# Kernel tuning notes

Measured on AMD Instinct MI355X. Metric: run time of the kernel, lower is better.

The kernel has to match this reference:

```python
import jax, jax.numpy as jnp
import numpy as np

N_NODES = 50000
N_EDGES = 600000
IN_CH, HID, EMB = 128, 128, 64


def _glorot(key, shape):
    fan_in, fan_out = shape[1], shape[0]
    lim = np.sqrt(6.0 / (fan_in + fan_out))
    return jax.random.uniform(key, shape, jnp.float32, -lim, lim)


def setup_inputs() -> dict:
    key = jax.random.key(0)
    ks = jax.random.split(key, 12)
    x = jax.random.normal(ks[0], (N_NODES, IN_CH), jnp.float32)
    edge_index = jax.random.randint(ks[1], (2, N_EDGES), 0, N_NODES, jnp.int64)
    return {
        "x": x,
        "edge_index": edge_index,
        # SAGEConv layer 1: lin_l (neighbor, with bias) + lin_r (root, no bias)
        "w1n": _glorot(ks[2], (HID, IN_CH)),
        "w1r": _glorot(ks[3], (HID, IN_CH)),
        "b1": jnp.zeros((HID,), jnp.float32),
        "w2n": _glorot(ks[4], (HID, HID)),
        "w2r": _glorot(ks[5], (HID, HID)),
        "b2": jnp.zeros((HID,), jnp.float32),
        "w3n": _glorot(ks[6], (EMB, HID)),
        "w3r": _glorot(ks[7], (EMB, HID)),
        "b3": jnp.zeros((EMB,), jnp.float32),
    }


def _sage_conv(x, src, dst, wn, wr, b):
    # mean aggregation of source-node features at destination nodes
    msg = x[src]                                            # [E, d_in]
    agg = jax.ops.segment_sum(msg, dst, num_segments=N_NODES)
    deg = jax.ops.segment_sum(jnp.ones((src.shape[0],), x.dtype), dst,
                              num_segments=N_NODES)
    agg = agg / jnp.maximum(deg, 1.0)[:, None]
    return agg @ wn.T + x @ wr.T + b


def reference(x, edge_index, w1n, w1r, b1, w2n, w2r, b2, w3n, w3r, b3):
    src, dst = edge_index[0], edge_index[1]
    h = jax.nn.relu(_sage_conv(x, src, dst, w1n, w1r, b1))
    # dropout(p=0.3) is identity in inference mode
    h = jax.nn.relu(_sage_conv(h, src, dst, w2n, w2r, b2))
    h = _sage_conv(h, src, dst, w3n, w3r, b3)
    return h
```

## Files before the change

kernel.cpp:

```cpp
#include <hip/hip_runtime.h>
#include <hip/hip_bf16.h>

#define NN 50000
#define ZROW 50000
#define ELLW 64
#define F8MINDEG 6

#define NB 128
#define BSH 9
#define BCAP 8192
#define EPB 2048

typedef short bf16x8 __attribute__((ext_vector_type(8)));
typedef float f32x4 __attribute__((ext_vector_type(4)));
typedef float floatx2 __attribute__((ext_vector_type(2)));

#if __has_builtin(__builtin_amdgcn_cvt_pk_f32_fp8) && __has_builtin(__builtin_amdgcn_cvt_pk_fp8_f32)
#define HWF8 1
#endif

__device__ __forceinline__ float bf_lo(unsigned int p) {
    union { unsigned int u; float f; } c; c.u = p << 16; return c.f;
}
__device__ __forceinline__ float bf_hi(unsigned int p) {
    union { unsigned int u; float f; } c; c.u = p & 0xffff0000u; return c.f;
}
__device__ __forceinline__ unsigned short bfbits(float f) {
    __hip_bfloat16 h = __float2bfloat16(f);
    union { __hip_bfloat16 b; unsigned short s; } c; c.b = h; return c.s;
}
__device__ __forceinline__ unsigned int pack_bf(float a, float b) {
    return (unsigned int)bfbits(a) | ((unsigned int)bfbits(b) << 16);
}
__device__ __forceinline__ void stv(float* p, float v) { *p = v; }
__device__ __forceinline__ void stv(unsigned short* p, float v) { *p = bfbits(v); }

__device__ __forceinline__ floatx2 bfpair(unsigned int p) {
    union { unsigned int u; float f; } lo, hi;
    lo.u = p << 16; hi.u = p & 0xffff0000u;
    return floatx2{lo.f, hi.f};
}
__device__ __forceinline__ void acc8v(const uint4& u, floatx2* a) {
    a[0] += bfpair(u.x); a[1] += bfpair(u.y);
    a[2] += bfpair(u.z); a[3] += bfpair(u.w);
}

__device__ __forceinline__ unsigned int enc1(float f) {
#ifdef HWF8
    return (unsigned int)__builtin_amdgcn_cvt_pk_fp8_f32(f, f, 0, false) & 0xffu;
#else
    union { float f; unsigned u; } c; c.f = f;
    unsigned s = (c.u >> 24) & 0x80u;
    float af = fabsf(f);
    if (af >= 448.f) return s | 0x7eu;
    if (af < 0.0078125f) {
        unsigned m = (unsigned)(af * 512.f + 0.5f);
        return s | (m > 7u ? 7u : m);
    }
    unsigned u = c.u & 0x7fffffffu;
    u += 0x7ffffu + ((u >> 20) & 1u);
    int e = (int)(u >> 23) - 120;
    if (e < 1) { unsigned m = (unsigned)(af * 512.f + 0.5f); return s | (m > 7u ? 7u : m); }
    if (e > 15) return s | 0x7eu;
    return s | ((unsigned)e << 3) | ((u >> 20) & 7u);
#endif
}
__device__ __forceinline__ unsigned int packf8_4(float x, float y, float z, float w) {
#ifdef HWF8
    int u = __builtin_amdgcn_cvt_pk_fp8_f32(x, y, 0, false);
    u = __builtin_amdgcn_cvt_pk_fp8_f32(z, w, u, true);
    return (unsigned int)u;
#else
    return enc1(x) | (enc1(y) << 8) | (enc1(z) << 16) | (enc1(w) << 24);
#endif
}
__device__ __forceinline__ void accf8v(const uint4& u, floatx2* a) {
#ifdef HWF8
    a[0] += __builtin_amdgcn_cvt_pk_f32_fp8(u.x, false);
    a[1] += __builtin_amdgcn_cvt_pk_f32_fp8(u.x, true);
    a[2] += __builtin_amdgcn_cvt_pk_f32_fp8(u.y, false);
    a[3] += __builtin_amdgcn_cvt_pk_f32_fp8(u.y, true);
    a[4] += __builtin_amdgcn_cvt_pk_f32_fp8(u.z, false);
    a[5] += __builtin_amdgcn_cvt_pk_f32_fp8(u.z, true);
    a[6] += __builtin_amdgcn_cvt_pk_f32_fp8(u.w, false);
    a[7] += __builtin_amdgcn_cvt_pk_f32_fp8(u.w, true);
#else
    const unsigned ww[4] = {u.x, u.y, u.z, u.w};
#pragma unroll
    for (int k = 0; k < 4; k++) {
#pragma unroll
        for (int j = 0; j < 4; j++) {
            unsigned b = (ww[k] >> (8 * j)) & 0xffu;
            unsigned v = ((b & 0x80u) << 24) | (((b & 0x7fu) + (120u << 3)) << 20);
            if ((b & 0x78u) == 0) v = 0u;
            union { unsigned u; float f; } c; c.u = v;
            a[(k * 4 + j) >> 1][(k * 4 + j) & 1] += c.f;
        }
    }
#endif
}

__global__ __launch_bounds__(256) void wb3z_kernel(
    const float* __restrict__ w1n, const float* __restrict__ w1r,
    const float* __restrict__ w2n, const float* __restrict__ w2r,
    const float* __restrict__ w3n, const float* __restrict__ w3r,
    unsigned short* __restrict__ wB1, unsigned short* __restrict__ wB2,
    unsigned short* __restrict__ wB3, int* __restrict__ zblk,
    unsigned short* __restrict__ xb, unsigned short* __restrict__ axc,
    unsigned short* __restrict__ h1b,
    unsigned char* __restrict__ xf8, unsigned char* __restrict__ h1f8) {
    int i = blockIdx.x * blockDim.x + threadIdx.x;
    if (i < 2048) zblk[i] = 0;
    int p = i - 2048;
    if (p >= 0 && p < 256) {
        if (p < 64)       ((unsigned int*)(xb  + (size_t)ZROW * 128))[p] = 0u;
        else if (p < 128) ((unsigned int*)(axc + (size_t)ZROW * 128))[p - 64] = 0u;
        else if (p < 192) ((unsigned int*)(h1b + (size_t)ZROW * 128))[p - 128] = 0u;
        else if (p < 224) ((unsigned int*)(xf8 + (size_t)ZROW * 128))[p - 192] = 0u;
        else              ((unsigned int*)(h1f8 + (size_t)ZROW * 128))[p - 224] = 0u;
    }
    if (i >= 12288) return;
    if (i < 8192) {
        const float* wn = (i < 4096) ? w1n : w2n;
        const float* wr = (i < 4096) ? w1r : w2r;
        unsigned short* wB = (i < 4096) ? wB1 : wB2;
        int li = i & 4095;
        int row = li >> 5;
        int j = (li & 31) * 4;
        float4 a = *(const float4*)(wn + (size_t)row * 128 + j);
        float4 b = *(const float4*)(wr + (size_t)row * 128 + j);
        *(uint2*)(wB + (size_t)row * 256 + j) = uint2{pack_bf(a.x, a.y), pack_bf(a.z, a.w)};
        *(uint2*)(wB + (size_t)row * 256 + 128 + j) = uint2{pack_bf(b.x, b.y), pack_bf(b.z, b.w)};
    } else {
        int li = i - 8192;
        const float* w = (li < 2048) ? w3n : w3r;
        int rbase = (li < 2048) ? 0 : 64;
        int lj = li & 2047;
        int row = lj >> 5;
        int j = (lj & 31) * 4;
        float4 a = *(const float4*)(w + (size_t)row * 128 + j);
        *(uint2*)(wB3 + (size_t)(rbase + row) * 128 + j) =
            uint2{pack_bf(a.x, a.y), pack_bf(a.z, a.w)};
    }
}

__global__ __launch_bounds__(256) void binify_cvt_kernel(
    const float* __restrict__ x,
    unsigned short* __restrict__ xb,
    unsigned char* __restrict__ xf8,
    const int* __restrict__ src,
    const int* __restrict__ dst,
    unsigned int* __restrict__ bpos,
    unsigned int* __restrict__ barr,
    int n4, int E, int nEB) {
    __shared__ int cnt[NB];
    __shared__ int gbase[NB];
    const int t = threadIdx.x;
    const int blk = blockIdx.x;
    if (blk < nEB) {
        int e0 = blk * EPB;
        int ss[8], dd[8], rr[8];
        bool v[8];
#pragma unroll
        for (int k = 0; k < 8; k++) {
            int e = e0 + t + (k << 8);
            v[k] = (e < E);
            ss[k] = v[k] ? src[e] : 0;
            dd[k] = v[k] ? dst[e] : 0;
            rr[k] = 0;
        }
        if (t < NB) cnt[t] = 0;
        __syncthreads();
#pragma unroll
        for (int k = 0; k < 8; k++)
            if (v[k]) rr[k] = atomicAdd(&cnt[dd[k] >> BSH], 1);
        __syncthreads();
        if (t < NB) {
            int c = cnt[t];
            gbase[t] = c ? (int)atomicAdd(&bpos[t], (unsigned)c) : 0;
        }
        __syncthreads();
#pragma unroll
        for (int k = 0; k < 8; k++) {
            if (v[k]) {
                int b = dd[k] >> BSH;
                int pos = gbase[b] + rr[k];
                if (pos < BCAP)
                    barr[b * BCAP + pos] =
                        (unsigned)ss[k] | ((unsigned)dd[k] << 16);
            }
        }
    }
    int gtid = blk * 256 + t;
    int gs = gridDim.x << 8;
    for (int i = gtid; i < n4; i += gs) {
        float4 vv = *(const float4*)(x + 4 * (size_t)i);
        *(uint2*)(xb + 4 * (size_t)i) = uint2{pack_bf(vv.x, vv.y), pack_bf(vv.z, vv.w)};
        *(unsigned int*)(xf8 + 4 * (size_t)i) = packf8_4(vv.x, vv.y, vv.z, vv.w);
    }
}

__global__ __launch_bounds__(256) void ellbuild_kernel(
    const unsigned int* __restrict__ bpos,
    const unsigned int* __restrict__ barr,
    unsigned short* __restrict__ ell,
    int* __restrict__ cnt) {
    __shared__ alignas(16) unsigned short lell[512 * 64];
    __shared__ int lcnt[512];
    const int t = threadIdx.x;
    const int b = blockIdx.x;
    const unsigned PADP = 0xC350C350u;
    for (int i = t; i < 4096; i += 256) ((uint4*)lell)[i] = uint4{PADP, PADP, PADP, PADP};
    for (int i = t; i < 512; i += 256) lcnt[i] = 0;
    __syncthreads();
    int ne = (int)bpos[b];
    if (ne > BCAP) ne = BCAP;
    const unsigned int* seg = barr + (size_t)b * BCAP;
    for (int i = t; i < ne; i += 256) {
        unsigned p = seg[i];
        int ln = (p >> 16) & 511;
        int r = atomicAdd(&lcnt[ln], 1);
        lell[(ln << 6) + (r & (ELLW - 1))] = (unsigned short)(p & 0xffffu);
    }
    __syncthreads();
    int node0 = b << BSH;
    int nn = NN - node0;
    if (nn > 512) nn = 512;
    if (nn <= 0) return;
    uint4* gell = (uint4*)(ell + (size_t)node0 * ELLW);
    const uint4* sell = (const uint4*)lell;
    for (int i = t; i < nn * 8; i += 256) gell[i] = sell[i];
    for (int i = t; i < nn; i += 256) cnt[node0 + i] = lcnt[i];
}

__global__ __launch_bounds__(256) void gather_kernel(
    const int* __restrict__ cnt, const unsigned short* __restrict__ ell,
    const unsigned char* __restrict__ hf8,
    const unsigned short* __restrict__ hb,
    unsigned short* __restrict__ axc,
    int n_nodes) {
    int tid = blockIdx.x * blockDim.x + threadIdx.x;
    int n = tid >> 3;
    if (n >= n_nodes) return;
    int c = (tid & 7) << 4;
    int deg = cnt[n];
    int dd8 = (min(deg, ELLW) + 7) & ~7;
    const unsigned short* cl = ell + (size_t)n * ELLW;
    floatx2 a[8];
#pragma unroll
    for (int k = 0; k < 8; k++) a[k] = floatx2{0.f, 0.f};
    if (deg >= F8MINDEG) {
        for (int i = 0; i < dd8; i += 8) {
            uint4 idv = *(const uint4*)(cl + i);
            int i0 = idv.x & 0xffff, i1 = idv.x >> 16;
            int i2 = idv.y & 0xffff, i3 = idv.y >> 16;
            int i4 = idv.z & 0xffff, i5 = idv.z >> 16;
            int i6 = idv.w & 0xffff, i7 = idv.w >> 16;
            uint4 u0 = *(const uint4*)(hf8 + (size_t)i0 * 128 + c);
            uint4 u1 = *(const uint4*)(hf8 + (size_t)i1 * 128 + c);
            uint4 u2 = *(const uint4*)(hf8 + (size_t)i2 * 128 + c);
            uint4 u3 = *(const uint4*)(hf8 + (size_t)i3 * 128 + c);
            uint4 u4 = *(const uint4*)(hf8 + (size_t)i4 * 128 + c);
            uint4 u5 = *(const uint4*)(hf8 + (size_t)i5 * 128 + c);
            uint4 u6 = *(const uint4*)(hf8 + (size_t)i6 * 128 + c);
            uint4 u7 = *(const uint4*)(hf8 + (size_t)i7 * 128 + c);
            accf8v(u0, a); accf8v(u1, a); accf8v(u2, a); accf8v(u3, a);
            accf8v(u4, a); accf8v(u5, a); accf8v(u6, a); accf8v(u7, a);
        }
    } else {
        for (int i = 0; i < dd8; i += 8) {
            uint4 idv = *(const uint4*)(cl + i);
            int is[8];
            is[0] = idv.x & 0xffff; is[1] = idv.x >> 16;
            is[2] = idv.y & 0xffff; is[3] = idv.y >> 16;
            is[4] = idv.z & 0xffff; is[5] = idv.z >> 16;
            is[6] = idv.w & 0xffff; is[7] = idv.w >> 16;
#pragma unroll
            for (int k = 0; k < 8; k++) {
                uint4 lo = *(const uint4*)(hb + (size_t)is[k] * 128 + c);
                uint4 hi = *(const uint4*)(hb + (size_t)is[k] * 128 + c + 8);
                acc8v(lo, a); acc8v(hi, a + 4);
            }
        }
    }
    float s = 1.0f / (float)max(deg, 1);
    uint4 p0 = {pack_bf(a[0][0] * s, a[0][1] * s), pack_bf(a[1][0] * s, a[1][1] * s),
                pack_bf(a[2][0] * s, a[2][1] * s), pack_bf(a[3][0] * s, a[3][1] * s)};
    uint4 p1 = {pack_bf(a[4][0] * s, a[4][1] * s), pack_bf(a[5][0] * s, a[5][1] * s),
                pack_bf(a[6][0] * s, a[6][1] * s), pack_bf(a[7][0] * s, a[7][1] * s)};
    *(uint4*)(axc + (size_t)n * 128 + c) = p0;
    *(uint4*)(axc + (size_t)n * 128 + c + 8) = p1;
}

__global__ __launch_bounds__(256) void gather_add_kernel(
    const int* __restrict__ cnt, const unsigned short* __restrict__ ell,
    const unsigned short* __restrict__ tu,
    const float* __restrict__ b3,
    float* __restrict__ out, int n_nodes) {
    int tid = blockIdx.x * blockDim.x + threadIdx.x;
    int n = tid >> 3;
    if (n >= n_nodes) return;
    int c = (tid & 7) << 3;
    int deg = cnt[n];
    int dd8 = (min(deg, ELLW) + 7) & ~7;
    const unsigned short* cl = ell + (size_t)n * ELLW;
    floatx2 a[4];
#pragma unroll
    for (int k = 0; k < 4; k++) a[k] = floatx2{0.f, 0.f};
    for (int i = 0; i < dd8; i += 8) {
        uint4 idv = *(const uint4*)(cl + i);
        int i0 = idv.x & 0xffff, i1 = idv.x >> 16;
        int i2 = idv.y & 0xffff, i3 = idv.y >> 16;
        int i4 = idv.z & 0xffff, i5 = idv.z >> 16;
        int i6 = idv.w & 0xffff, i7 = idv.w >> 16;
        uint4 u0 = *(const uint4*)(tu + (size_t)i0 * 128 + c);
        uint4 u1 = *(const uint4*)(tu + (size_t)i1 * 128 + c);
        uint4 u2 = *(const uint4*)(tu + (size_t)i2 * 128 + c);
        uint4 u3 = *(const uint4*)(tu + (size_t)i3 * 128 + c);
        uint4 u4 = *(const uint4*)(tu + (size_t)i4 * 128 + c);
        uint4 u5 = *(const uint4*)(tu + (size_t)i5 * 128 + c);
        uint4 u6 = *(const uint4*)(tu + (size_t)i6 * 128 + c);
        uint4 u7 = *(const uint4*)(tu + (size_t)i7 * 128 + c);
        acc8v(u0, a); acc8v(u1, a); acc8v(u2, a); acc8v(u3, a);
        acc8v(u4, a); acc8v(u5, a); acc8v(u6, a); acc8v(u7, a);
    }
    float s = 1.0f / (float)max(deg, 1);
    uint4 uu = *(const uint4*)(tu + (size_t)n * 128 + 64 + c);
    float4 bA = *(const float4*)(b3 + c);
    float4 bB = *(const float4*)(b3 + c + 4);
    float* o = out + (size_t)n * 64 + c;
    o[0] = a[0][0] * s + bf_lo(uu.x) + bA.x;
    o[1] = a[0][1] * s + bf_hi(uu.x) + bA.y;
    o[2] = a[1][0] * s + bf_lo(uu.y) + bA.z;
    o[3] = a[1][1] * s + bf_hi(uu.y) + bA.w;
    o[4] = a[2][0] * s + bf_lo(uu.z) + bB.x;
    o[5] = a[2][1] * s + bf_hi(uu.z) + bB.y;
    o[6] = a[3][0] * s + bf_lo(uu.w) + bB.z;
    o[7] = a[3][1] * s + bf_hi(uu.w) + bB.w;
}

template <int NKS, bool RELU, bool BIAS, bool F8, typename OUT_T>
__global__ __launch_bounds__(256) void mfma_gemm(
    const unsigned short* __restrict__ A0, const unsigned short* __restrict__ A1,
    const unsigned short* __restrict__ B,
    const float* __restrict__ bias,
    OUT_T* __restrict__ out, unsigned char* __restrict__ f8out,
    int M, int N, int nTilesN) {
    constexpr int KTOT = NKS * 64;
    constexpr int LDB = KTOT + 8;
    __shared__ unsigned short As[2][128 * 72];
    __shared__ unsigned short Bs[64 * LDB];
    const int t = threadIdx.x;
    const int w = t >> 6, l = t & 63;
    const int tileM = blockIdx.x / nTilesN;
    const int n0 = (blockIdx.x - tileM * nTilesN) * 64;
    const int m0 = tileM * 128;
    const int lr = l & 15, lq = l >> 4;

    for (int c = t; c < 64 * (KTOT / 8); c += 256) {
        int row = c / (KTOT / 8);
        int ko = (c - row * (KTOT / 8)) * 8;
        *(uint4*)(&Bs[row * LDB + ko]) =
            *(const uint4*)(&B[(size_t)(n0 + row) * KTOT + ko]);
    }
    for (int c = t; c < 1024; c += 256) {
        int row = c >> 3;
        int ko = (c & 7) * 8;
        int gm = m0 + row;
        uint4 v = {0u, 0u, 0u, 0u};
        if (gm < M) v = *(const uint4*)(A0 + (size_t)gm * 128 + ko);
        *(uint4*)(&As[0][row * 72 + ko]) = v;
    }
    __syncthreads();

    f32x4 acc[2][4];
#pragma unroll
    for (int tm = 0; tm < 2; tm++)
#pragma unroll
        for (int tn = 0; tn < 4; tn++) acc[tm][tn] = f32x4{0.f, 0.f, 0.f, 0.f};

#pragma unroll
    for (int ks = 0; ks < NKS; ks++) {
        uint4 pf[4];
        if (ks + 1 < NKS) {
            int ns = ks + 1;
            const unsigned short* Asrc = (ns < NKS / 2)
                ? (A0 + (size_t)ns * 64) : (A1 + (size_t)(ns - NKS / 2) * 64);
#pragma unroll
            for (int j = 0; j < 4; j++) {
                int c = t + j * 256;
                int row = c >> 3;
                int ko = (c & 7) * 8;
                int gm = m0 + row;
                pf[j] = uint4{0u, 0u, 0u, 0u};
                if (gm < M) pf[j] = *(const uint4*)(Asrc + (size_t)gm * 128 + ko);
            }
        }
        const unsigned short* as = As[ks & 1];
#pragma unroll
        for (int kc = 0; kc < 2; kc++) {
            int lk = kc * 32 + lq * 8;
            bf16x8 af[2], bfr[4];
            af[0] = *(const bf16x8*)(&as[(w * 32 + lr) * 72 + lk]);
            af[1] = *(const bf16x8*)(&as[(w * 32 + 16 + lr) * 72 + lk]);
#pragma unroll
            for (int tn = 0; tn < 4; tn++)
                bfr[tn] = *(const bf16x8*)(&Bs[(tn * 16 + lr) * LDB + ks * 64 + lk]);
#pragma unroll
            for (int tm = 0; tm < 2; tm++)
#pragma unroll
                for (int tn = 0; tn < 4; tn++)
                    acc[tm][tn] = __builtin_amdgcn_mfma_f32_16x16x32_bf16(
                        af[tm], bfr[tn], acc[tm][tn], 0, 0, 0);
        }
        if (ks + 1 < NKS) {
#pragma unroll
            for (int j = 0; j < 4; j++) {
                int c = t + j * 256;
                int row = c >> 3;
                int ko = (c & 7) * 8;
                *(uint4*)(&As[(ks + 1) & 1][row * 72 + ko]) = pf[j];
            }
            __syncthreads();
        }
    }

#pragma unroll
    for (int tn = 0; tn < 4; tn++) {
        int n = n0 + tn * 16 + lr;
        float bj = BIAS ? bias[n] : 0.f;
#pragma unroll
        for (int tm = 0; tm < 2; tm++) {
#pragma unroll
            for (int i = 0; i < 4; i++) {
                int m = m0 + w * 32 + tm * 16 + lq * 4 + i;
                if (m < M) {
                    float v = acc[tm][tn][i] + bj;
                    if (RELU) v = fmaxf(v, 0.f);
                    stv(&out[(size_t)m * N + n], v);
                    if (F8) f8out[(size_t)m * N + n] = (unsigned char)enc1(v);
                }
            }
        }
    }
}

extern "C" void kernel_launch(void* const* d_in, const int* in_sizes, int n_in,
                              void* d_out, int out_size, void* d_ws, size_t ws_size,
                              hipStream_t stream) {
    const float* x  = (const float*)d_in[0];
    const int* ei   = (const int*)d_in[1];
    const float* w1n = (const float*)d_in[2];
    const float* w1r = (const float*)d_in[3];
    const float* b1  = (const float*)d_in[4];
    const float* w2n = (const float*)d_in[5];
    const float* w2r = (const float*)d_in[6];
    const float* b2  = (const float*)d_in[7];
    const float* w3n = (const float*)d_in[8];
    const float* w3r = (const float*)d_in[9];
    const float* b3  = (const float*)d_in[10];
    float* out = (float*)d_out;

    const int E = in_sizes[1] / 2;
    const int* src = ei;
    const int* dst = ei + E;

    char* ws = (char*)d_ws;
    unsigned short* xb  = (unsigned short*)(ws);
    unsigned short* axc = (unsigned short*)(ws + 13000000);
    unsigned short* h1b = (unsigned short*)(ws + 26000000);
    unsigned short* h2b = (unsigned short*)(ws + 39000000);
    unsigned int* barr  = (unsigned int*)(ws + 39000000);
    unsigned short* ell = (unsigned short*)(ws + 52000000);
    int* cnt            = (int*)  (ws + 64800000);
    int* zblk           = (int*)  (ws + 65400000);
    unsigned int* bpos  = (unsigned int*)(zblk + 1536);
    unsigned short* wB1 = (unsigned short*)(ws + 65500000);
    unsigned short* wB2 = (unsigned short*)(ws + 65600000);
    unsigned short* wB3 = (unsigned short*)(ws + 65700000);
    unsigned char* xf8  = (unsigned char*)(ws + 65800000);
    unsigned char* h1f8 = (unsigned char*)(ws + 72300000);

    const int nEB = (E + EPB - 1) / EPB;

    wb3z_kernel<<<48, 256, 0, stream>>>(
        w1n, w1r, w2n, w2r, w3n, w3r, wB1, wB2, wB3, zblk, xb, axc, h1b, xf8, h1f8);
    binify_cvt_kernel<<<2048, 256, 0, stream>>>(x, xb, xf8, src, dst,
                                                bpos, barr, NN * 32, E, nEB);
    ellbuild_kernel<<<(NN + 511) / 512, 256, 0, stream>>>(bpos, barr, ell, cnt);

    const int gatherBlocks = (NN * 8 + 255) / 256;
    const int mTiles = (NN + 127) / 128;

    gather_kernel<<<gatherBlocks, 256, 0, stream>>>(cnt, ell, xf8, xb, axc, NN);
    mfma_gemm<4, true, true, true, unsigned short>
        <<<mTiles * 2, 256, 0, stream>>>(axc, xb, wB1, b1, h1b, h1f8, NN, 128, 2);

    gather_kernel<<<gatherBlocks, 256, 0, stream>>>(cnt, ell, h1f8, h1b, axc, NN);
    mfma_gemm<4, true, true, false, unsigned short>
        <<<mTiles * 2, 256, 0, stream>>>(axc, h1b, wB2, b2, h2b, nullptr, NN, 128, 2);

    mfma_gemm<2, false, false, false, unsigned short>
        <<<mTiles * 2, 256, 0, stream>>>(h2b, h2b + 64, wB3, nullptr, axc, nullptr,
                                         NN, 128, 2);
    gather_add_kernel<<<gatherBlocks, 256, 0, stream>>>(
        cnt, ell, axc, b3, out, NN);
}
```

Measured before the change: 230.9 us.

## Widen GEMM tile to full 128 output columns and stream weights per k-step

Each GEMM block now computes all 128 output columns instead of 64, which halves the grid and means each A row-tile is loaded once rather than twice. The weight matrix is no longer staged whole in shared memory. It is double-buffered per 64-wide k-slice alongside A. This roughly halves global A traffic and block count, at the cost of doubling accumulator registers per thread (occupancy risk) and adding per-step B loads.

```diff
diff --git a/kernel.cpp b/kernel.cpp
--- a/kernel.cpp
+++ b/kernel.cpp
@@ -345,43 +345,37 @@
     const unsigned short* __restrict__ B,
     const float* __restrict__ bias,
     OUT_T* __restrict__ out, unsigned char* __restrict__ f8out,
-    int M, int N, int nTilesN) {
+    int M) {
     constexpr int KTOT = NKS * 64;
-    constexpr int LDB = KTOT + 8;
     __shared__ unsigned short As[2][128 * 72];
-    __shared__ unsigned short Bs[64 * LDB];
+    __shared__ unsigned short Bs[2][128 * 72];
     const int t = threadIdx.x;
     const int w = t >> 6, l = t & 63;
-    const int tileM = blockIdx.x / nTilesN;
-    const int n0 = (blockIdx.x - tileM * nTilesN) * 64;
-    const int m0 = tileM * 128;
+    const int m0 = blockIdx.x * 128;
     const int lr = l & 15, lq = l >> 4;
 
-    for (int c = t; c < 64 * (KTOT / 8); c += 256) {
-        int row = c / (KTOT / 8);
-        int ko = (c - row * (KTOT / 8)) * 8;
-        *(uint4*)(&Bs[row * LDB + ko]) =
-            *(const uint4*)(&B[(size_t)(n0 + row) * KTOT + ko]);
-    }
-    for (int c = t; c < 1024; c += 256) {
+#pragma unroll
+    for (int j = 0; j < 4; j++) {
+        int c = t + j * 256;
         int row = c >> 3;
         int ko = (c & 7) * 8;
         int gm = m0 + row;
-        uint4 v = {0u, 0u, 0u, 0u};
-        if (gm < M) v = *(const uint4*)(A0 + (size_t)gm * 128 + ko);
-        *(uint4*)(&As[0][row * 72 + ko]) = v;
+        uint4 va = {0u, 0u, 0u, 0u};
+        if (gm < M) va = *(const uint4*)(A0 + (size_t)gm * 128 + ko);
+        *(uint4*)(&As[0][row * 72 + ko]) = va;
+        *(uint4*)(&Bs[0][row * 72 + ko]) = *(const uint4*)(B + (size_t)row * KTOT + ko);
     }
     __syncthreads();
 
-    f32x4 acc[2][4];
+    f32x4 acc[2][8];
 #pragma unroll
     for (int tm = 0; tm < 2; tm++)
 #pragma unroll
-        for (int tn = 0; tn < 4; tn++) acc[tm][tn] = f32x4{0.f, 0.f, 0.f, 0.f};
+        for (int tn = 0; tn < 8; tn++) acc[tm][tn] = f32x4{0.f, 0.f, 0.f, 0.f};
 
 #pragma unroll
     for (int ks = 0; ks < NKS; ks++) {
-        uint4 pf[4];
+        uint4 pfA[4], pfB[4];
         if (ks + 1 < NKS) {
             int ns = ks + 1;
             const unsigned short* Asrc = (ns < NKS / 2)
@@ -392,24 +386,26 @@
                 int row = c >> 3;
                 int ko = (c & 7) * 8;
                 int gm = m0 + row;
-                pf[j] = uint4{0u, 0u, 0u, 0u};
-                if (gm < M) pf[j] = *(const uint4*)(Asrc + (size_t)gm * 128 + ko);
+                pfA[j] = uint4{0u, 0u, 0u, 0u};
+                if (gm < M) pfA[j] = *(const uint4*)(Asrc + (size_t)gm * 128 + ko);
+                pfB[j] = *(const uint4*)(B + (size_t)row * KTOT + ns * 64 + ko);
             }
         }
         const unsigned short* as = As[ks & 1];
+        const unsigned short* bs = Bs[ks & 1];
 #pragma unroll
         for (int kc = 0; kc < 2; kc++) {
             int lk = kc * 32 + lq * 8;
-            bf16x8 af[2], bfr[4];
+            bf16x8 af[2], bfr[8];
             af[0] = *(const bf16x8*)(&as[(w * 32 + lr) * 72 + lk]);
             af[1] = *(const bf16x8*)(&as[(w * 32 + 16 + lr) * 72 + lk]);
 #pragma unroll
-            for (int tn = 0; tn < 4; tn++)
-                bfr[tn] = *(const bf16x8*)(&Bs[(tn * 16 + lr) * LDB + ks * 64 + lk]);
+            for (int tn = 0; tn < 8; tn++)
+                bfr[tn] = *(const bf16x8*)(&bs[(tn * 16 + lr) * 72 + lk]);
 #pragma unroll
             for (int tm = 0; tm < 2; tm++)
 #pragma unroll
-                for (int tn = 0; tn < 4; tn++)
+                for (int tn = 0; tn < 8; tn++)
                     acc[tm][tn] = __builtin_amdgcn_mfma_f32_16x16x32_bf16(
                         af[tm], bfr[tn], acc[tm][tn], 0, 0, 0);
         }
@@ -419,15 +415,16 @@
                 int c = t + j * 256;
                 int row = c >> 3;
                 int ko = (c & 7) * 8;
-                *(uint4*)(&As[(ks + 1) & 1][row * 72 + ko]) = pf[j];
+                *(uint4*)(&As[(ks + 1) & 1][row * 72 + ko]) = pfA[j];
+                *(uint4*)(&Bs[(ks + 1) & 1][row * 72 + ko]) = pfB[j];
             }
             __syncthreads();
         }
     }
 
 #pragma unroll
-    for (int tn = 0; tn < 4; tn++) {
-        int n = n0 + tn * 16 + lr;
+    for (int tn = 0; tn < 8; tn++) {
+        int n = tn * 16 + lr;
         float bj = BIAS ? bias[n] : 0.f;
 #pragma unroll
         for (int tm = 0; tm < 2; tm++) {
@@ -437,8 +434,8 @@
                 if (m < M) {
                     float v = acc[tm][tn][i] + bj;
                     if (RELU) v = fmaxf(v, 0.f);
-                    stv(&out[(size_t)m * N + n], v);
-                    if (F8) f8out[(size_t)m * N + n] = (unsigned char)enc1(v);
+                    stv(&out[(size_t)m * 128 + n], v);
+                    if (F8) f8out[(size_t)m * 128 + n] = (unsigned char)enc1(v);
                 }
             }
         }
@@ -494,15 +491,14 @@
 
     gather_kernel<<<gatherBlocks, 256, 0, stream>>>(cnt, ell, xf8, xb, axc, NN);
     mfma_gemm<4, true, true, true, unsigned short>
-        <<<mTiles * 2, 256, 0, stream>>>(axc, xb, wB1, b1, h1b, h1f8, NN, 128, 2);
+        <<<mTiles, 256, 0, stream>>>(axc, xb, wB1, b1, h1b, h1f8, NN);
 
     gather_kernel<<<gatherBlocks, 256, 0, stream>>>(cnt, ell, h1f8, h1b, axc, NN);
     mfma_gemm<4, true, true, false, unsigned short>
-        <<<mTiles * 2, 256, 0, stream>>>(axc, h1b, wB2, b2, h2b, nullptr, NN, 128, 2);
+        <<<mTiles, 256, 0, stream>>>(axc, h1b, wB2, b2, h2b, nullptr, NN);
 
     mfma_gemm<2, false, false, false, unsigned short>
-        <<<mTiles * 2, 256, 0, stream>>>(h2b, h2b + 64, wB3, nullptr, axc, nullptr,
-                                         NN, 128, 2);
+        <<<mTiles, 256, 0, stream>>>(h2b, h2b + 64, wB3, nullptr, axc, nullptr, NN);
     gather_add_kernel<<<gatherBlocks, 256, 0, stream>>>(
         cnt, ell, axc, b3, out, NN);
 }
```

New measurement: 221.0 us. 4.3% less time.
